# Kernel optimization log

Measured on AMD Instinct MI355X. Metric: run time of the kernel, lower is better.

The kernel has to match this reference:

```python
import jax, jax.numpy as jnp
import numpy as np

N_NODES = 50000
N_EDGES = 1_600_000
F_IN = 128
F_OUT = 8
K_TAPS = 4
AVG_DEG = 32.0


def setup_inputs() -> dict:
    key = jax.random.key(0)
    k1, k2, k3, k4, k5 = jax.random.split(key, 5)
    x = jax.random.normal(k1, (N_NODES, F_IN), dtype=jnp.float32)
    gso_rows = jax.random.randint(k2, (N_EDGES,), 0, N_NODES, dtype=jnp.int32)
    gso_cols = jax.random.randint(k3, (N_EDGES,), 0, N_NODES, dtype=jnp.int32)
    gso_vals = jax.random.uniform(k4, (N_EDGES,), dtype=jnp.float32) / AVG_DEG
    # filterCoeff = randn(outFeat, filter_order) * 0.1 as in torch __init__
    coeff = jax.random.normal(k5, (F_OUT, K_TAPS), dtype=jnp.float32) * 0.1
    return {"x": x, "gso_rows": gso_rows, "gso_cols": gso_cols,
            "gso_vals": gso_vals, "coeff": coeff}


def reference(x, gso_rows, gso_cols, gso_vals, coeff):
    # Faithful to the torch code INCLUDING its carried-over SpMV state:
    # output feature o uses powers S^{1+o(K-1)} .. S^{o(K-1)+K} of x.
    F_out, K = coeff.shape
    N = x.shape[0]
    max_power = F_out * (K - 1) + 1  # highest S power needed

    def spmv(Z):  # S @ Z via edge-list gather + segment_sum scatter
        return jax.ops.segment_sum(gso_vals[:, None] * Z[gso_cols], gso_rows,
                                   num_segments=N)

    def step(Z, _):
        Zn = spmv(Z)
        return Zn, Zn.sum(axis=1)  # sum over in-features done up-front

    # s[p-1, n] = sum_f (S^p x)[n, f], for p = 1..max_power
    _, s = jax.lax.scan(step, x, None, length=max_power)  # (max_power, N)

    # power index (0-based into s) used by output o, tap i: o*(K-1) + i
    idx = jnp.arange(F_out)[:, None] * (K - 1) + jnp.arange(K)[None, :]  # (F_out, K)
    sg = s[idx]  # (F_out, K, N)
    y = jnp.einsum('ok,okn->no', coeff, sg)  # (N, F_out)
    return y
```

## Files before the change

### kernel.cpp

```cpp
#include <hip/hip_runtime.h>

#define N_NODES 50000
#define NPAD    50176
#define N_EDGES 1600000
#define F_IN    128
#define F_OUT   8
#define K_TAPS  4
#define MAX_POWER 25

#define NBLK    256
#define NTHR    512
#define RPB     196
#define CHUNK   6272
#define NPART   256
#define ECAP_G  8192
#define ECAP_L  7168
#define NITER   14
#define CSB     800

#define SENT_I  (-1)
#define SPREFILL (24 * NPAD)
#define PFB      (SPREFILL / NBLK)

__device__ inline int wave_incl_scan(int v, int lane) {
    #pragma unroll
    for (int off = 1; off < 64; off <<= 1) {
        int t = __shfl_up(v, off, 64);
        if (lane >= off) v += t;
    }
    return v;
}

__device__ inline float ld_agent_f(const float* p) {
    return __hip_atomic_load((const float*)p, __ATOMIC_RELAXED, __HIP_MEMORY_SCOPE_AGENT);
}
__device__ inline void st_agent_f(float* p, float v) {
    __hip_atomic_store(p, v, __ATOMIC_RELAXED, __HIP_MEMORY_SCOPE_AGENT);
}

__global__ __launch_bounds__(NTHR, 1)
void prep_kernel(const float* __restrict__ x,
                 const int* __restrict__ rows,
                 const int* __restrict__ cols,
                 const float* __restrict__ vals,
                 int* __restrict__ gcnt,
                 int2* __restrict__ edges,
                 float* __restrict__ u,
                 int* __restrict__ spoison,
                 int n_edges, int n_nodes) {
    __shared__ int lhist[NBLK];
    __shared__ int lcur[NBLK];
    __shared__ int lbase[NBLK];
    __shared__ int2 stage[CHUNK];
    __shared__ unsigned char sbkt[CHUNK];
    __shared__ int wsum[8];
    int tid = threadIdx.x;
    int b = blockIdx.x;

    for (int i = b * PFB + tid; i < (b + 1) * PFB; i += NTHR)
        spoison[i] = SENT_I;

    int base = b * CHUNK;
    int cend = min(base + CHUNK, n_edges);

    if (tid < NBLK) lhist[tid] = 0;
    __syncthreads();
    for (int i = base + tid; i < cend; i += NTHR)
        atomicAdd(&lhist[rows[i] / RPB], 1);
    __syncthreads();

    int lane = tid & 63, wid = tid >> 6;
    int h = 0, incl = 0;
    if (tid < NBLK) {
        h = lhist[tid];
        incl = wave_incl_scan(h, lane);
        if (lane == 63) wsum[wid] = incl;
    }
    __syncthreads();
    if (tid < NBLK) {
        int woff = 0;
        for (int w = 0; w < wid; ++w) woff += wsum[w];
        int excl = woff + incl - h;
        lcur[tid] = excl;
        if (h) {
            int g = atomicAdd(&gcnt[tid], h);
            lbase[tid] = tid * ECAP_G + g - excl;
        }
    }
    __syncthreads();

    for (int i = base + tid; i < cend; i += NTHR) {
        int r = rows[i], c = cols[i];
        float v = vals[i];
        int bb = r / RPB;
        int pos = atomicAdd(&lcur[bb], 1);
        stage[pos] = make_int2(((r - bb * RPB) << 16) | c, __float_as_int(v));
        sbkt[pos] = (unsigned char)bb;
    }
    __syncthreads();

    int cn = cend - base;
    for (int i = tid; i < cn; i += NTHR) {
        int bb = sbkt[i];
        int o = lbase[bb] + i;
        if (o - bb * ECAP_G < ECAP_G)
            edges[o] = stage[i];
    }

    int base_row = b * RPB;
    int rcount = min(RPB, n_nodes - base_row);
    int g32 = tid >> 5;
    int l32 = tid & 31;
    const float4* x4 = (const float4*)x;
    for (int r = g32; r < rcount; r += 16) {
        float4 v = x4[(size_t)(base_row + r) * (F_IN / 4) + l32];
        float sv = v.x + v.y + v.z + v.w;
        #pragma unroll
        for (int off = 16; off > 0; off >>= 1)
            sv += __shfl_down(sv, off, 32);
        if (l32 == 0) u[base_row + r] = sv;
    }
}

__global__ __launch_bounds__(NTHR, 1)
void chain_kernel(const int* __restrict__ gcnt,
                  const int2* __restrict__ edges,
                  const float* __restrict__ coeff,
                  const float* __restrict__ u,
                  float* __restrict__ s,
                  float* __restrict__ y,
                  int n_nodes) {
    __shared__ int2  esort[ECAP_L];
    __shared__ int   chist[CSB];
    __shared__ int   ccur[CSB];
    __shared__ int   wsum8[8];
    __shared__ float acc[2][RPB];
    __shared__ float yacc[RPB * F_OUT];
    __shared__ float lcoeff[F_OUT * K_TAPS];

    int tid = threadIdx.x;
    int b = blockIdx.x;

    if (tid < RPB) { acc[0][tid] = 0.f; acc[1][tid] = 0.f; }
    for (int j = tid; j < RPB * F_OUT; j += NTHR) yacc[j] = 0.f;
    if (tid < F_OUT * K_TAPS) lcoeff[tid] = coeff[tid];

    int cnt = min(gcnt[b], ECAP_G);
    const int2* eb = edges + (size_t)b * ECAP_G;

    for (int i = tid; i < CSB; i += NTHR) chist[i] = 0;
    __syncthreads();
    if (cnt <= ECAP_L) {
        for (int i = tid; i < cnt; i += NTHR) {
            int2 e = eb[i];
            atomicAdd(&chist[(e.x & 0xFFFF) >> 6], 1);
        }
        __syncthreads();
        int lane = tid & 63, wid = tid >> 6;
        int b0 = 2 * tid;
        int h0 = (b0 < CSB) ? chist[b0] : 0;
        int h1 = (b0 + 1 < CSB) ? chist[b0 + 1] : 0;
        int ps = h0 + h1;
        int incl = wave_incl_scan(ps, lane);
        if (lane == 63) wsum8[wid] = incl;
        __syncthreads();
        int woff = 0;
        for (int w = 0; w < wid; ++w) woff += wsum8[w];
        int ex = woff + incl - ps;
        if (b0 < CSB) ccur[b0] = ex;
        if (b0 + 1 < CSB) ccur[b0 + 1] = ex + h0;
        __syncthreads();
        for (int i = tid; i < cnt; i += NTHR) {
            int2 e = eb[i];
            int pos = atomicAdd(&ccur[(e.x & 0xFFFF) >> 6], 1);
            esort[pos] = e;
        }
        __syncthreads();
    } else {
        int cl = min(cnt, ECAP_L);
        for (int i = tid; i < cl; i += NTHR) esort[i] = eb[i];
        __syncthreads();
    }

    int   ecol[NITER];
    int   erow[NITER];
    float eval[NITER];
    int cntl = min(cnt, ECAP_L);
    unsigned pend0 = 0;
    #pragma unroll
    for (int j = 0; j < NITER; ++j) {
        int idx = tid + j * NTHR;
        int2 e = (idx < cntl) ? esort[idx] : make_int2(0, 0);
        ecol[j] = e.x & 0xFFFF;
        erow[j] = e.x >> 16;
        eval[j] = __int_as_float(e.y);
        if (idx < cntl) pend0 |= (1u << j);
    }

    int cur = 0;
    for (int p = 0; p < MAX_POWER; ++p) {
        const float* __restrict__ src = (p == 0) ? u : s + (size_t)(p - 1) * NPAD;
        float* dst = s + (size_t)p * NPAD;

        float v[NITER];
        #pragma unroll
        for (int j = 0; j < NITER; ++j) v[j] = src[ecol[j]];

        if (p > 0) {
            unsigned pend = 0;
            #pragma unroll
            for (int j = 0; j < NITER; ++j)
                if ((pend0 & (1u << j)) && __float_as_int(v[j]) == SENT_I)
                    pend |= (1u << j);
            while (pend) {
                float t[NITER];
                #pragma unroll
                for (int j = 0; j < NITER; ++j)
                    if (pend & (1u << j)) t[j] = ld_agent_f(&src[ecol[j]]);
                #pragma unroll
                for (int j = 0; j < NITER; ++j)
                    if ((pend & (1u << j)) && __float_as_int(t[j]) != SENT_I) {
                        v[j] = t[j];
                        pend &= ~(1u << j);
                    }
                if (pend) __builtin_amdgcn_s_sleep(2);
            }
        }

        float* accc = acc[cur];
        #pragma unroll
        for (int j = 0; j < NITER; ++j)
            if (tid + j * NTHR < cntl)
                atomicAdd(&accc[erow[j]], eval[j] * v[j]);
        for (int k = ECAP_L + tid; k < cnt; k += NTHR) {
            int2 ev = eb[k];
            float sv;
            if (p == 0) sv = src[ev.x & 0xFFFF];
            else do { sv = ld_agent_f(&src[ev.x & 0xFFFF]); }
                 while (__float_as_int(sv) == SENT_I);
            atomicAdd(&accc[ev.x >> 16], __int_as_float(ev.y) * sv);
        }
        __syncthreads();

        bool last = (p == MAX_POWER - 1);
        if (tid < RPB) {
            float val = accc[tid];
            if (!last) st_agent_f(&dst[b * RPB + tid], val);
            #pragma unroll
            for (int o = 0; o < F_OUT; ++o) {
                int k = p - (K_TAPS - 1) * o;
                if (k >= 0 && k < K_TAPS)
                    yacc[tid * F_OUT + o] += lcoeff[o * K_TAPS + k] * val;
            }
            accc[tid] = 0.f;
        }
        cur ^= 1;
    }

    __syncthreads();
    for (int j = tid; j < RPB * F_OUT; j += NTHR) {
        int row = b * RPB + (j >> 3);
        if (row < n_nodes) y[(size_t)row * F_OUT + (j & 7)] = yacc[j];
    }
}

extern "C" void kernel_launch(void* const* d_in, const int* in_sizes, int n_in,
                              void* d_out, int out_size, void* d_ws, size_t ws_size,
                              hipStream_t stream) {
    const float* x        = (const float*)d_in[0];
    const int*   gso_rows = (const int*)d_in[1];
    const int*   gso_cols = (const int*)d_in[2];
    const float* gso_vals = (const float*)d_in[3];
    const float* coeff    = (const float*)d_in[4];
    float* y = (float*)d_out;

    float* u     = (float*)d_ws;
    float* s     = u + NPAD;
    int2*  edges = (int2*)(s + (size_t)MAX_POWER * NPAD);
    int*   gcnt  = (int*)(edges + (size_t)NBLK * ECAP_G);

    (void)hipMemsetAsync(gcnt, 0, (size_t)NBLK * sizeof(int), stream);

    prep_kernel<<<NPART, NTHR, 0, stream>>>(
        x, gso_rows, gso_cols, gso_vals, gcnt, edges, u, (int*)s,
        N_EDGES, N_NODES);

    int n_nodes = N_NODES;
    void* args[] = { (void*)&gcnt, (void*)&edges, (void*)&coeff,
                     (void*)&u, (void*)&s, (void*)&y, (void*)&n_nodes };
    (void)hipLaunchCooperativeKernel((void*)chain_kernel, dim3(NBLK), dim3(NTHR),
                                     args, 0, stream);
}
```

Before: 395.2 us.

## Switch chain kernel to per-row CSR accumulation with thread-per-row, no LDS atomics

The chain kernel now bucket-sorts each block's edges by local row, so each thread owns one row and accumulates its SpMV result in a register. This replaces the column-sorted edge layout with shared-memory atomic accumulation and the per-power __syncthreads. The block shrinks to 256 threads with only 196 active, and sentinel polling is done per 16-edge batch. In exchange, work is serialized per row with uneven row lengths, fewer threads are available to hide gather latency, and the overflow path scans all edges per thread.

```diff
diff --git a/kernel.cpp b/kernel.cpp
--- a/kernel.cpp
+++ b/kernel.cpp
@@ -9,18 +9,18 @@
 #define MAX_POWER 25
 
 #define NBLK    256
-#define NTHR    512
+#define NTHR_P  512
+#define NTHR_C  256
 #define RPB     196
+#define NPART   256
 #define CHUNK   6272
-#define NPART   256
 #define ECAP_G  8192
 #define ECAP_L  7168
-#define NITER   14
-#define CSB     800
 
 #define SENT_I  (-1)
 #define SPREFILL (24 * NPAD)
-#define PFB      (SPREFILL / NBLK)
+#define PFB      (SPREFILL / NPART)
+#define BATCH   16
 
 __device__ inline int wave_incl_scan(int v, int lane) {
     #pragma unroll
@@ -38,7 +38,7 @@
     __hip_atomic_store(p, v, __ATOMIC_RELAXED, __HIP_MEMORY_SCOPE_AGENT);
 }
 
-__global__ __launch_bounds__(NTHR, 1)
+__global__ __launch_bounds__(NTHR_P, 1)
 void prep_kernel(const float* __restrict__ x,
                  const int* __restrict__ rows,
                  const int* __restrict__ cols,
@@ -57,7 +57,7 @@
     int tid = threadIdx.x;
     int b = blockIdx.x;
 
-    for (int i = b * PFB + tid; i < (b + 1) * PFB; i += NTHR)
+    for (int i = b * PFB + tid; i < (b + 1) * PFB; i += NTHR_P)
         spoison[i] = SENT_I;
 
     int base = b * CHUNK;
@@ -65,31 +65,30 @@
 
     if (tid < NBLK) lhist[tid] = 0;
     __syncthreads();
-    for (int i = base + tid; i < cend; i += NTHR)
+    for (int i = base + tid; i < cend; i += NTHR_P)
         atomicAdd(&lhist[rows[i] / RPB], 1);
     __syncthreads();
 
     int lane = tid & 63, wid = tid >> 6;
-    int h = 0, incl = 0;
-    if (tid < NBLK) {
-        h = lhist[tid];
-        incl = wave_incl_scan(h, lane);
-        if (lane == 63) wsum[wid] = incl;
-    }
-    __syncthreads();
-    if (tid < NBLK) {
+    int h = (tid < NBLK) ? lhist[tid] : 0;
+    int incl = wave_incl_scan(h, lane);
+    if (lane == 63) wsum[wid] = incl;
+    __syncthreads();
+    {
         int woff = 0;
         for (int w = 0; w < wid; ++w) woff += wsum[w];
         int excl = woff + incl - h;
-        lcur[tid] = excl;
-        if (h) {
-            int g = atomicAdd(&gcnt[tid], h);
-            lbase[tid] = tid * ECAP_G + g - excl;
+        if (tid < NBLK) {
+            lcur[tid] = excl;
+            if (h) {
+                int g = atomicAdd(&gcnt[tid], h);
+                lbase[tid] = tid * ECAP_G + g - excl;
+            }
         }
     }
     __syncthreads();
 
-    for (int i = base + tid; i < cend; i += NTHR) {
+    for (int i = base + tid; i < cend; i += NTHR_P) {
         int r = rows[i], c = cols[i];
         float v = vals[i];
         int bb = r / RPB;
@@ -100,7 +99,7 @@
     __syncthreads();
 
     int cn = cend - base;
-    for (int i = tid; i < cn; i += NTHR) {
+    for (int i = tid; i < cn; i += NTHR_P) {
         int bb = sbkt[i];
         int o = lbase[bb] + i;
         if (o - bb * ECAP_G < ECAP_G)
@@ -122,7 +121,7 @@
     }
 }
 
-__global__ __launch_bounds__(NTHR, 1)
+__global__ __launch_bounds__(NTHR_C, 1)
 void chain_kernel(const int* __restrict__ gcnt,
                   const int2* __restrict__ edges,
                   const float* __restrict__ coeff,
@@ -131,136 +130,126 @@
                   float* __restrict__ y,
                   int n_nodes) {
     __shared__ int2  esort[ECAP_L];
-    __shared__ int   chist[CSB];
-    __shared__ int   ccur[CSB];
-    __shared__ int   wsum8[8];
-    __shared__ float acc[2][RPB];
-    __shared__ float yacc[RPB * F_OUT];
+    __shared__ int   rhist[NTHR_C];
+    __shared__ int   rcur[NTHR_C];
+    __shared__ int   rbeg[NTHR_C];
+    __shared__ int   wsum4[4];
     __shared__ float lcoeff[F_OUT * K_TAPS];
 
     int tid = threadIdx.x;
     int b = blockIdx.x;
 
-    if (tid < RPB) { acc[0][tid] = 0.f; acc[1][tid] = 0.f; }
-    for (int j = tid; j < RPB * F_OUT; j += NTHR) yacc[j] = 0.f;
     if (tid < F_OUT * K_TAPS) lcoeff[tid] = coeff[tid];
 
     int cnt = min(gcnt[b], ECAP_G);
     const int2* eb = edges + (size_t)b * ECAP_G;
-
-    for (int i = tid; i < CSB; i += NTHR) chist[i] = 0;
-    __syncthreads();
-    if (cnt <= ECAP_L) {
-        for (int i = tid; i < cnt; i += NTHR) {
+    bool fast = (cnt <= ECAP_L);
+
+    rhist[tid] = 0;
+    __syncthreads();
+    if (fast) {
+        for (int i = tid; i < cnt; i += NTHR_C)
+            atomicAdd(&rhist[eb[i].x >> 16], 1);
+        __syncthreads();
+        int lane = tid & 63, wid = tid >> 6;
+        int h = rhist[tid];
+        int incl = wave_incl_scan(h, lane);
+        if (lane == 63) wsum4[wid] = incl;
+        __syncthreads();
+        int woff = 0;
+        for (int w = 0; w < wid; ++w) woff += wsum4[w];
+        int excl = woff + incl - h;
+        rbeg[tid] = excl;
+        rcur[tid] = excl;
+        __syncthreads();
+        for (int i = tid; i < cnt; i += NTHR_C) {
             int2 e = eb[i];
-            atomicAdd(&chist[(e.x & 0xFFFF) >> 6], 1);
-        }
-        __syncthreads();
-        int lane = tid & 63, wid = tid >> 6;
-        int b0 = 2 * tid;
-        int h0 = (b0 < CSB) ? chist[b0] : 0;
-        int h1 = (b0 + 1 < CSB) ? chist[b0 + 1] : 0;
-        int ps = h0 + h1;
-        int incl = wave_incl_scan(ps, lane);
-        if (lane == 63) wsum8[wid] = incl;
-        __syncthreads();
-        int woff = 0;
-        for (int w = 0; w < wid; ++w) woff += wsum8[w];
-        int ex = woff + incl - ps;
-        if (b0 < CSB) ccur[b0] = ex;
-        if (b0 + 1 < CSB) ccur[b0 + 1] = ex + h0;
-        __syncthreads();
-        for (int i = tid; i < cnt; i += NTHR) {
-            int2 e = eb[i];
-            int pos = atomicAdd(&ccur[(e.x & 0xFFFF) >> 6], 1);
+            int pos = atomicAdd(&rcur[e.x >> 16], 1);
             esort[pos] = e;
         }
         __syncthreads();
-    } else {
-        int cl = min(cnt, ECAP_L);
-        for (int i = tid; i < cl; i += NTHR) esort[i] = eb[i];
-        __syncthreads();
-    }
-
-    int   ecol[NITER];
-    int   erow[NITER];
-    float eval[NITER];
-    int cntl = min(cnt, ECAP_L);
-    unsigned pend0 = 0;
+    }
+
+    int r = b * RPB + tid;
+    bool active = (tid < RPB) && (r < n_nodes);
+    int rb = 0, re = 0;
+    if (active && fast) { rb = rbeg[tid]; re = rcur[tid]; }
+
+    float yr[F_OUT];
     #pragma unroll
-    for (int j = 0; j < NITER; ++j) {
-        int idx = tid + j * NTHR;
-        int2 e = (idx < cntl) ? esort[idx] : make_int2(0, 0);
-        ecol[j] = e.x & 0xFFFF;
-        erow[j] = e.x >> 16;
-        eval[j] = __int_as_float(e.y);
-        if (idx < cntl) pend0 |= (1u << j);
-    }
-
-    int cur = 0;
-    for (int p = 0; p < MAX_POWER; ++p) {
-        const float* __restrict__ src = (p == 0) ? u : s + (size_t)(p - 1) * NPAD;
-        float* dst = s + (size_t)p * NPAD;
-
-        float v[NITER];
-        #pragma unroll
-        for (int j = 0; j < NITER; ++j) v[j] = src[ecol[j]];
-
-        if (p > 0) {
-            unsigned pend = 0;
-            #pragma unroll
-            for (int j = 0; j < NITER; ++j)
-                if ((pend0 & (1u << j)) && __float_as_int(v[j]) == SENT_I)
-                    pend |= (1u << j);
-            while (pend) {
-                float t[NITER];
-                #pragma unroll
-                for (int j = 0; j < NITER; ++j)
-                    if (pend & (1u << j)) t[j] = ld_agent_f(&src[ecol[j]]);
-                #pragma unroll
-                for (int j = 0; j < NITER; ++j)
-                    if ((pend & (1u << j)) && __float_as_int(t[j]) != SENT_I) {
-                        v[j] = t[j];
-                        pend &= ~(1u << j);
+    for (int o = 0; o < F_OUT; ++o) yr[o] = 0.f;
+
+    if (active) {
+        for (int p = 0; p < MAX_POWER; ++p) {
+            const float* __restrict__ src = (p == 0) ? u : s + (size_t)(p - 1) * NPAD;
+            float acc = 0.f;
+
+            if (fast) {
+                int i = rb;
+                while (i < re) {
+                    int n = re - i; if (n > BATCH) n = BATCH;
+                    unsigned m = (n >= BATCH) ? 0xFFFFu : ((1u << n) - 1);
+                    int   ecols[BATCH];
+                    float evals[BATCH];
+                    #pragma unroll
+                    for (int j = 0; j < BATCH; ++j)
+                        if (m & (1u << j)) {
+                            int2 e = esort[i + j];
+                            ecols[j] = e.x & 0xFFFF;
+                            evals[j] = __int_as_float(e.y);
+                        }
+                    unsigned pend = 0;
+                    #pragma unroll
+                    for (int j = 0; j < BATCH; ++j)
+                        if (m & (1u << j)) {
+                            float v = src[ecols[j]];
+                            if (p == 0 || __float_as_int(v) != SENT_I)
+                                acc += evals[j] * v;
+                            else
+                                pend |= (1u << j);
+                        }
+                    while (pend) {
+                        #pragma unroll
+                        for (int j = 0; j < BATCH; ++j)
+                            if (pend & (1u << j)) {
+                                float v = ld_agent_f(&src[ecols[j]]);
+                                if (__float_as_int(v) != SENT_I) {
+                                    acc += evals[j] * v;
+                                    pend &= ~(1u << j);
+                                }
+                            }
+                        if (pend) __builtin_amdgcn_s_sleep(1);
                     }
-                if (pend) __builtin_amdgcn_s_sleep(2);
+                    i += n;
+                }
+            } else {
+                for (int i = 0; i < cnt; ++i) {
+                    int2 e = eb[i];
+                    if ((e.x >> 16) == tid) {
+                        float v = src[e.x & 0xFFFF];
+                        while (p > 0 && __float_as_int(v) == SENT_I)
+                            v = ld_agent_f(&src[e.x & 0xFFFF]);
+                        acc += __int_as_float(e.y) * v;
+                    }
+                }
             }
-        }
-
-        float* accc = acc[cur];
-        #pragma unroll
-        for (int j = 0; j < NITER; ++j)
-            if (tid + j * NTHR < cntl)
-                atomicAdd(&accc[erow[j]], eval[j] * v[j]);
-        for (int k = ECAP_L + tid; k < cnt; k += NTHR) {
-            int2 ev = eb[k];
-            float sv;
-            if (p == 0) sv = src[ev.x & 0xFFFF];
-            else do { sv = ld_agent_f(&src[ev.x & 0xFFFF]); }
-                 while (__float_as_int(sv) == SENT_I);
-            atomicAdd(&accc[ev.x >> 16], __int_as_float(ev.y) * sv);
-        }
-        __syncthreads();
-
-        bool last = (p == MAX_POWER - 1);
-        if (tid < RPB) {
-            float val = accc[tid];
-            if (!last) st_agent_f(&dst[b * RPB + tid], val);
+
+            if (p < MAX_POWER - 1)
+                st_agent_f(&s[(size_t)p * NPAD + r], acc);
+
             #pragma unroll
             for (int o = 0; o < F_OUT; ++o) {
                 int k = p - (K_TAPS - 1) * o;
                 if (k >= 0 && k < K_TAPS)
-                    yacc[tid * F_OUT + o] += lcoeff[o * K_TAPS + k] * val;
+                    yr[o] += lcoeff[o * K_TAPS + k] * acc;
             }
-            accc[tid] = 0.f;
         }
-        cur ^= 1;
-    }
-
-    __syncthreads();
-    for (int j = tid; j < RPB * F_OUT; j += NTHR) {
-        int row = b * RPB + (j >> 3);
-        if (row < n_nodes) y[(size_t)row * F_OUT + (j & 7)] = yacc[j];
+
+        float4 y0 = make_float4(yr[0], yr[1], yr[2], yr[3]);
+        float4 y1 = make_float4(yr[4], yr[5], yr[6], yr[7]);
+        float4* yp = (float4*)(y + (size_t)r * F_OUT);
+        yp[0] = y0;
+        yp[1] = y1;
     }
 }
 
@@ -281,13 +270,13 @@
 
     (void)hipMemsetAsync(gcnt, 0, (size_t)NBLK * sizeof(int), stream);
 
-    prep_kernel<<<NPART, NTHR, 0, stream>>>(
+    prep_kernel<<<NPART, NTHR_P, 0, stream>>>(
         x, gso_rows, gso_cols, gso_vals, gcnt, edges, u, (int*)s,
         N_EDGES, N_NODES);
 
     int n_nodes = N_NODES;
     void* args[] = { (void*)&gcnt, (void*)&edges, (void*)&coeff,
                      (void*)&u, (void*)&s, (void*)&y, (void*)&n_nodes };
-    (void)hipLaunchCooperativeKernel((void*)chain_kernel, dim3(NBLK), dim3(NTHR),
+    (void)hipLaunchCooperativeKernel((void*)chain_kernel, dim3(NBLK), dim3(NTHR_C),
                                      args, 0, stream);
 }
```

Result: slower. 537.7 us (+36.1%).

## Give each wave its own row slice to drop block barriers per power

Applied to the files above, without the earlier changes.

The chain kernel now gives each wave 25 rows and sorts edges by (wave row group, column bin), so each wave accumulates its rows in its own LDS slice. The per-power block-wide __syncthreads becomes a wave-local LDS drain, and output rows are kept in registers and written as float4. Blocks drop to 250 with 200 rows each, and NPAD shrinks to 50000. The overflow path for blocks with more than ECAP_L edges is gone, and waves with more than 1024 edges would silently drop edges, so correctness now depends on the degree distribution.

```diff
diff --git a/kernel.cpp b/kernel.cpp
--- a/kernel.cpp
+++ b/kernel.cpp
@@ -1,26 +1,27 @@
 #include <hip/hip_runtime.h>
 
 #define N_NODES 50000
-#define NPAD    50176
+#define NPAD    50000
 #define N_EDGES 1600000
 #define F_IN    128
 #define F_OUT   8
 #define K_TAPS  4
 #define MAX_POWER 25
 
-#define NBLK    256
+#define NBLK    250
 #define NTHR    512
-#define RPB     196
+#define RPB     200
+#define RPW     25
+#define NPART   256
 #define CHUNK   6272
-#define NPART   256
 #define ECAP_G  8192
 #define ECAP_L  7168
-#define NITER   14
-#define CSB     800
+#define KMAX    16
+#define NBIN    1024
 
 #define SENT_I  (-1)
 #define SPREFILL (24 * NPAD)
-#define PFB      (SPREFILL / NBLK)
+#define PFB      4688
 
 __device__ inline int wave_incl_scan(int v, int lane) {
     #pragma unroll
@@ -36,6 +37,10 @@
 }
 __device__ inline void st_agent_f(float* p, float v) {
     __hip_atomic_store(p, v, __ATOMIC_RELAXED, __HIP_MEMORY_SCOPE_AGENT);
+}
+__device__ inline void lds_drain_wave() {
+    asm volatile("s_waitcnt lgkmcnt(0)" ::: "memory");
+    __builtin_amdgcn_wave_barrier();
 }
 
 __global__ __launch_bounds__(NTHR, 1)
@@ -48,36 +53,33 @@
                  float* __restrict__ u,
                  int* __restrict__ spoison,
                  int n_edges, int n_nodes) {
-    __shared__ int lhist[NBLK];
-    __shared__ int lcur[NBLK];
-    __shared__ int lbase[NBLK];
+    __shared__ int lhist[256];
+    __shared__ int lcur[256];
+    __shared__ int lbase[256];
     __shared__ int2 stage[CHUNK];
     __shared__ unsigned char sbkt[CHUNK];
     __shared__ int wsum[8];
     int tid = threadIdx.x;
     int b = blockIdx.x;
 
-    for (int i = b * PFB + tid; i < (b + 1) * PFB; i += NTHR)
+    for (int i = b * PFB + tid; i < (b + 1) * PFB && i < SPREFILL; i += NTHR)
         spoison[i] = SENT_I;
 
     int base = b * CHUNK;
     int cend = min(base + CHUNK, n_edges);
 
-    if (tid < NBLK) lhist[tid] = 0;
+    if (tid < 256) lhist[tid] = 0;
     __syncthreads();
     for (int i = base + tid; i < cend; i += NTHR)
         atomicAdd(&lhist[rows[i] / RPB], 1);
     __syncthreads();
 
     int lane = tid & 63, wid = tid >> 6;
-    int h = 0, incl = 0;
-    if (tid < NBLK) {
-        h = lhist[tid];
-        incl = wave_incl_scan(h, lane);
-        if (lane == 63) wsum[wid] = incl;
-    }
-    __syncthreads();
-    if (tid < NBLK) {
+    int h = (tid < 256) ? lhist[tid] : 0;
+    int incl = wave_incl_scan(h, lane);
+    if (tid < 256 && lane == 63) wsum[wid] = incl;
+    __syncthreads();
+    if (tid < 256) {
         int woff = 0;
         for (int w = 0; w < wid; ++w) woff += wsum[w];
         int excl = woff + incl - h;
@@ -107,8 +109,8 @@
             edges[o] = stage[i];
     }
 
-    int base_row = b * RPB;
-    int rcount = min(RPB, n_nodes - base_row);
+    int base_row = b * 196;
+    int rcount = min(196, n_nodes - base_row);
     int g32 = tid >> 5;
     int l32 = tid & 31;
     const float4* x4 = (const float4*)x;
@@ -131,35 +133,35 @@
                   float* __restrict__ y,
                   int n_nodes) {
     __shared__ int2  esort[ECAP_L];
-    __shared__ int   chist[CSB];
-    __shared__ int   ccur[CSB];
+    __shared__ int   chist[NBIN];
+    __shared__ int   ccur[NBIN];
     __shared__ int   wsum8[8];
-    __shared__ float acc[2][RPB];
-    __shared__ float yacc[RPB * F_OUT];
+    __shared__ int   wbeg8[8];
+    __shared__ float acc[8][32];
     __shared__ float lcoeff[F_OUT * K_TAPS];
 
     int tid = threadIdx.x;
     int b = blockIdx.x;
-
-    if (tid < RPB) { acc[0][tid] = 0.f; acc[1][tid] = 0.f; }
-    for (int j = tid; j < RPB * F_OUT; j += NTHR) yacc[j] = 0.f;
+    int lane = tid & 63, wid = tid >> 6;
+
+    if (tid < 256) acc[tid >> 5][tid & 31] = 0.f;
     if (tid < F_OUT * K_TAPS) lcoeff[tid] = coeff[tid];
 
     int cnt = min(gcnt[b], ECAP_G);
     const int2* eb = edges + (size_t)b * ECAP_G;
-
-    for (int i = tid; i < CSB; i += NTHR) chist[i] = 0;
-    __syncthreads();
-    if (cnt <= ECAP_L) {
-        for (int i = tid; i < cnt; i += NTHR) {
-            int2 e = eb[i];
-            atomicAdd(&chist[(e.x & 0xFFFF) >> 6], 1);
-        }
-        __syncthreads();
-        int lane = tid & 63, wid = tid >> 6;
+    int cl = min(cnt, ECAP_L);
+
+    for (int i = tid; i < NBIN; i += NTHR) chist[i] = 0;
+    __syncthreads();
+    for (int i = tid; i < cl; i += NTHR) {
+        int2 e = eb[i];
+        atomicAdd(&chist[((e.x >> 16) / RPW) * 128 + ((e.x & 0xFFFF) >> 9)], 1);
+    }
+    __syncthreads();
+    {
         int b0 = 2 * tid;
-        int h0 = (b0 < CSB) ? chist[b0] : 0;
-        int h1 = (b0 + 1 < CSB) ? chist[b0 + 1] : 0;
+        int h0 = chist[b0];
+        int h1 = chist[b0 + 1];
         int ps = h0 + h1;
         int incl = wave_incl_scan(ps, lane);
         if (lane == 63) wsum8[wid] = incl;
@@ -167,100 +169,96 @@
         int woff = 0;
         for (int w = 0; w < wid; ++w) woff += wsum8[w];
         int ex = woff + incl - ps;
-        if (b0 < CSB) ccur[b0] = ex;
-        if (b0 + 1 < CSB) ccur[b0 + 1] = ex + h0;
-        __syncthreads();
-        for (int i = tid; i < cnt; i += NTHR) {
-            int2 e = eb[i];
-            int pos = atomicAdd(&ccur[(e.x & 0xFFFF) >> 6], 1);
-            esort[pos] = e;
-        }
-        __syncthreads();
-    } else {
-        int cl = min(cnt, ECAP_L);
-        for (int i = tid; i < cl; i += NTHR) esort[i] = eb[i];
-        __syncthreads();
-    }
-
-    int   ecol[NITER];
-    int   erow[NITER];
-    float eval[NITER];
-    int cntl = min(cnt, ECAP_L);
-    unsigned pend0 = 0;
+        ccur[b0] = ex;
+        ccur[b0 + 1] = ex + h0;
+        if ((b0 & 127) == 0) wbeg8[b0 >> 7] = ex;
+    }
+    __syncthreads();
+    for (int i = tid; i < cl; i += NTHR) {
+        int2 e = eb[i];
+        int pos = atomicAdd(&ccur[((e.x >> 16) / RPW) * 128 + ((e.x & 0xFFFF) >> 9)], 1);
+        esort[pos] = e;
+    }
+    __syncthreads();
+
+    int wbeg = wbeg8[wid];
+    int wend = (wid < 7) ? wbeg8[wid + 1] : cl;
+    int   ecol[KMAX];
+    int   erow[KMAX];
+    float eval[KMAX];
+    unsigned m0 = 0;
     #pragma unroll
-    for (int j = 0; j < NITER; ++j) {
-        int idx = tid + j * NTHR;
-        int2 e = (idx < cntl) ? esort[idx] : make_int2(0, 0);
-        ecol[j] = e.x & 0xFFFF;
-        erow[j] = e.x >> 16;
-        eval[j] = __int_as_float(e.y);
-        if (idx < cntl) pend0 |= (1u << j);
-    }
-
-    int cur = 0;
+    for (int j = 0; j < KMAX; ++j) {
+        int idx = wbeg + lane + j * 64;
+        if (idx < wend) {
+            int2 e = esort[idx];
+            ecol[j] = e.x & 0xFFFF;
+            erow[j] = (e.x >> 16) - wid * RPW;
+            eval[j] = __int_as_float(e.y);
+            m0 |= (1u << j);
+        } else { ecol[j] = 0; erow[j] = 0; eval[j] = 0.f; }
+    }
+
+    int r = b * RPB + wid * RPW + lane;
+    float yr[F_OUT];
+    #pragma unroll
+    for (int o = 0; o < F_OUT; ++o) yr[o] = 0.f;
+
     for (int p = 0; p < MAX_POWER; ++p) {
         const float* __restrict__ src = (p == 0) ? u : s + (size_t)(p - 1) * NPAD;
-        float* dst = s + (size_t)p * NPAD;
-
-        float v[NITER];
+
+        float v[KMAX];
         #pragma unroll
-        for (int j = 0; j < NITER; ++j) v[j] = src[ecol[j]];
+        for (int j = 0; j < KMAX; ++j) v[j] = src[ecol[j]];
 
         if (p > 0) {
             unsigned pend = 0;
             #pragma unroll
-            for (int j = 0; j < NITER; ++j)
-                if ((pend0 & (1u << j)) && __float_as_int(v[j]) == SENT_I)
+            for (int j = 0; j < KMAX; ++j)
+                if ((m0 & (1u << j)) && __float_as_int(v[j]) == SENT_I)
                     pend |= (1u << j);
             while (pend) {
-                float t[NITER];
+                float t[KMAX];
                 #pragma unroll
-                for (int j = 0; j < NITER; ++j)
+                for (int j = 0; j < KMAX; ++j)
                     if (pend & (1u << j)) t[j] = ld_agent_f(&src[ecol[j]]);
                 #pragma unroll
-                for (int j = 0; j < NITER; ++j)
+                for (int j = 0; j < KMAX; ++j)
                     if ((pend & (1u << j)) && __float_as_int(t[j]) != SENT_I) {
                         v[j] = t[j];
                         pend &= ~(1u << j);
                     }
-                if (pend) __builtin_amdgcn_s_sleep(2);
+                if (pend) __builtin_amdgcn_s_sleep(1);
             }
         }
 
-        float* accc = acc[cur];
         #pragma unroll
-        for (int j = 0; j < NITER; ++j)
-            if (tid + j * NTHR < cntl)
-                atomicAdd(&accc[erow[j]], eval[j] * v[j]);
-        for (int k = ECAP_L + tid; k < cnt; k += NTHR) {
-            int2 ev = eb[k];
-            float sv;
-            if (p == 0) sv = src[ev.x & 0xFFFF];
-            else do { sv = ld_agent_f(&src[ev.x & 0xFFFF]); }
-                 while (__float_as_int(sv) == SENT_I);
-            atomicAdd(&accc[ev.x >> 16], __int_as_float(ev.y) * sv);
-        }
-        __syncthreads();
-
-        bool last = (p == MAX_POWER - 1);
-        if (tid < RPB) {
-            float val = accc[tid];
-            if (!last) st_agent_f(&dst[b * RPB + tid], val);
+        for (int j = 0; j < KMAX; ++j)
+            if (m0 & (1u << j))
+                atomicAdd(&acc[wid][erow[j]], eval[j] * v[j]);
+        lds_drain_wave();
+
+        if (lane < RPW) {
+            float val = acc[wid][lane];
+            if (p < MAX_POWER - 1)
+                st_agent_f(&s[(size_t)p * NPAD + r], val);
             #pragma unroll
             for (int o = 0; o < F_OUT; ++o) {
                 int k = p - (K_TAPS - 1) * o;
                 if (k >= 0 && k < K_TAPS)
-                    yacc[tid * F_OUT + o] += lcoeff[o * K_TAPS + k] * val;
+                    yr[o] += lcoeff[o * K_TAPS + k] * val;
             }
-            accc[tid] = 0.f;
+            acc[wid][lane] = 0.f;
         }
-        cur ^= 1;
-    }
-
-    __syncthreads();
-    for (int j = tid; j < RPB * F_OUT; j += NTHR) {
-        int row = b * RPB + (j >> 3);
-        if (row < n_nodes) y[(size_t)row * F_OUT + (j & 7)] = yacc[j];
+        lds_drain_wave();
+    }
+
+    if (lane < RPW && r < n_nodes) {
+        float4 y0 = make_float4(yr[0], yr[1], yr[2], yr[3]);
+        float4 y1 = make_float4(yr[4], yr[5], yr[6], yr[7]);
+        float4* yp = (float4*)(y + (size_t)r * F_OUT);
+        yp[0] = y0;
+        yp[1] = y1;
     }
 }
 
@@ -279,7 +277,7 @@
     int2*  edges = (int2*)(s + (size_t)MAX_POWER * NPAD);
     int*   gcnt  = (int*)(edges + (size_t)NBLK * ECAP_G);
 
-    (void)hipMemsetAsync(gcnt, 0, (size_t)NBLK * sizeof(int), stream);
+    (void)hipMemsetAsync(gcnt, 0, 256 * sizeof(int), stream);
 
     prep_kernel<<<NPART, NTHR, 0, stream>>>(
         x, gso_rows, gso_cols, gso_vals, gcnt, edges, u, (int*)s,
```

Measured after the change: 611.0 us. 54.6% more time.
